# Kernel tuning notes

Measured on AMD Instinct MI355X. Metric: run time of the kernel, lower is better.

Reference implementation:

```python
import jax, jax.numpy as jnp
import numpy as np

L = 8          # fixed number of instance labels (0 = background), all assumed present
DV = 0.5       # delta_v
DD = 1.5       # delta_d
LOSS_WEIGHT = 1.0


def _safe_norm(x, axis):
    sq = jnp.sum(x * x, axis=axis)
    pos = sq > 0
    return jnp.sqrt(jnp.where(pos, sq, 1.0)) * pos.astype(x.dtype)


def _per_image(emb, inst, kern, tmask):
    # emb: [D,H,W], inst: [H,W] int, kern/tmask: [H,W] float
    D, H, W = emb.shape
    HW = H * W
    tm = (tmask > 0.5).astype(inst.dtype)
    kb = (kern > 0.5).astype(inst.dtype)
    inst = inst * tm
    inst_k = (inst * kb).reshape(-1)          # kernel-region labels
    inst_f = inst.reshape(-1)                 # full-region labels
    emb_f = emb.reshape(D, -1).T              # [HW, D]

    # --- generate_coef: first/second occurrence (row-major) of each label ---
    flat = jnp.arange(HW)
    eq = inst_f[None, :] == jnp.arange(L)[:, None]          # [L, HW]
    idxs = jnp.where(eq, flat[None, :], HW)
    first = jnp.min(idxs, axis=1)
    second = jnp.min(jnp.where(idxs == first[:, None], HW, idxs), axis=1)
    first = jnp.minimum(first, HW - 1)
    second = jnp.minimum(second, HW - 1)
    r0, c0 = first // W, first % W
    r1, c1 = second // W, second % W
    # pos_id = (tmp[0,0], tmp[1,0], tmp[0,-1], tmp[1,-1]) as in the source
    pos = jnp.stack([r0, r1, c0, c1], axis=1).astype(jnp.float32)  # [L,4]
    diag = jnp.sqrt(jnp.float32(H * H + W * W))
    coef_diag = jnp.exp(jnp.sqrt((pos[:, 0] - pos[:, 2]) ** 2 +
                                 (pos[:, 1] - pos[:, 3]) ** 2) / diag / 2.0)
    zmask = (jnp.arange(L) > 0).astype(jnp.float32)          # skip label 0
    coef_diag = coef_diag * zmask
    s = pos[:, 0] + pos[:, 2]
    t = pos[:, 1] + pos[:, 3]
    dp = jnp.sqrt((s[:, None] - s[None, :]) ** 2 + (t[:, None] - t[None, :]) ** 2)
    coef_off = 1.0 - 20.0 * jnp.exp(-4.0 - 2.5 * dp / diag)
    eye = jnp.eye(L, dtype=bool)
    coef = jnp.where(eye, coef_diag[:, None], coef_off)
    coef = coef * zmask[:, None] * zmask[None, :]

    # --- per-label kernel means (segment mean) ---
    ones = jnp.ones((HW,), jnp.float32)
    cnt_k = jax.ops.segment_sum(ones, inst_k, num_segments=L)
    mean = jax.ops.segment_sum(emb_f, inst_k, num_segments=L)
    mean = mean / jnp.maximum(cnt_k, 1.0)[:, None]           # [L, D]
    mean = mean * zmask[:, None]

    # --- l_agg: per-pixel distance to own-label mean, segment-mean per label ---
    mean_px = mean[inst_f]                                   # [HW, D] gather
    dist = _safe_norm(emb_f - mean_px, axis=1)
    cd_px = coef_diag[inst_f]
    val = jnp.log(jax.nn.relu(cd_px * dist - DV) ** 2 + 1.0)
    cnt = jax.ops.segment_sum(ones, inst_f, num_segments=L)
    l_agg_per = jax.ops.segment_sum(val, inst_f, num_segments=L) / jnp.maximum(cnt, 1.0)
    l_agg = jnp.mean(l_agg_per[1:])

    # --- l_dis: coefficient-weighted pairwise hinge between means ---
    Dn = _safe_norm(mean[:, None, :] - mean[None, :, :], axis=-1)  # [L, L]
    pm = (~eye) & (zmask[:, None] > 0) & (zmask[None, :] > 0)
    vals = jnp.log(jax.nn.relu(2.0 * DD - coef * Dn) ** 2 + 1.0)
    l_dis = jnp.sum(jnp.where(pm, vals, 0.0)) / ((L - 1) * (L - 2))

    # --- l_reg ---
    l_reg = jnp.mean(jnp.log(_safe_norm(mean, axis=1) + 1.0)) * 0.001
    return l_agg + l_dis + l_reg


def reference(emb, instance, kernel, training_mask, bboxes):
    # bboxes is accepted but unused, matching the original forward_single
    loss_batch = jax.vmap(_per_image)(emb, instance, kernel, training_mask)
    return LOSS_WEIGHT * jnp.mean(loss_batch)


def setup_inputs() -> dict:
    key = jax.random.key(0)
    k1, k2, k3, k4, k5 = jax.random.split(key, 5)
    B, D, H, W = 8, 4, 640, 640
    emb = jax.random.normal(k1, (B, D, H, W), dtype=jnp.float32)
    instance = jax.random.randint(k2, (B, H, W), 0, L, dtype=jnp.int32)
    kernel = jax.random.uniform(k3, (B, H, W), dtype=jnp.float32)
    training_mask = jax.random.uniform(k4, (B, H, W), dtype=jnp.float32)
    bboxes = jax.random.uniform(k5, (B, 10, 4), dtype=jnp.float32)
    return {"emb": emb, "instance": instance, "kernel": kernel,
            "training_mask": training_mask, "bboxes": bboxes}
```

## Files before the change

kernel.cpp:

```cpp
#include <hip/hip_runtime.h>
#include <hip/hip_bf16.h>

#define B_   8
#define D_   4
#define H_   640
#define W_   640
#define HW_  (H_ * W_)
#define L_   8
#define NL   (L_ - 1)
#define BLOCK 256
#define ITER  8

__device__ __forceinline__ void gatom_add(float* p, float v) {
    unsafeAtomicAdd(p, v);
}

__global__ void k_init(int* firstIdx, int* secondIdx, float* fbuf) {
    int t = threadIdx.x;
    if (t < B_ * L_) { firstIdx[t] = HW_; secondIdx[t] = HW_; }
    for (int i = t; i < 448; i += blockDim.x) fbuf[i] = 0.0f;
}

__global__ __launch_bounds__(BLOCK) void k_pass1(
        const float* __restrict__ emb, const int* __restrict__ inst,
        const float* __restrict__ kern, const float* __restrict__ tmask,
        int* __restrict__ firstIdx, int* __restrict__ secondIdx,
        float* __restrict__ cntk, float* __restrict__ cntf,
        float* __restrict__ sumemb) {
    __shared__ float sCntF[L_], sCntK[L_], sSum[L_ * D_];
    __shared__ int   sM1[L_], sM2[L_];

    const int tid = threadIdx.x;
    if (tid < L_) { sCntF[tid] = 0.f; sCntK[tid] = 0.f; sM1[tid] = HW_; sM2[tid] = HW_; }
    if (tid < L_ * D_) sSum[tid] = 0.f;
    __syncthreads();

    const int b    = blockIdx.y;
    const int base = b * HW_;

    float cf[NL], ck[NL], sm[NL][D_];
    int   m1[NL], m2[NL];
    #pragma unroll
    for (int l = 0; l < NL; ++l) {
        cf[l] = 0.f; ck[l] = 0.f; m1[l] = HW_; m2[l] = HW_;
        #pragma unroll
        for (int d = 0; d < D_; ++d) sm[l][d] = 0.f;
    }

    #pragma unroll
    for (int it = 0; it < ITER; ++it) {
        int p = blockIdx.x * (BLOCK * ITER) + it * BLOCK + tid;
        int lab  = inst[base + p];
        float tm = tmask[base + p];
        float kn = kern[base + p];
        int lf = (tm > 0.5f) ? lab : 0;
        bool kb = (kn > 0.5f);
        float e0 = emb[(b * D_ + 0) * HW_ + p];
        float e1 = emb[(b * D_ + 1) * HW_ + p];
        float e2 = emb[(b * D_ + 2) * HW_ + p];
        float e3 = emb[(b * D_ + 3) * HW_ + p];

        #pragma unroll
        for (int l = 1; l < L_; ++l) {
            const int k = l - 1;
            bool pf = (lf == l);
            cf[k] += pf ? 1.0f : 0.0f;
            float mk = (pf && kb) ? 1.0f : 0.0f;
            ck[k] += mk;
            sm[k][0] += mk * e0;
            sm[k][1] += mk * e1;
            sm[k][2] += mk * e2;
            sm[k][3] += mk * e3;
            bool t1 = pf && (m1[k] == HW_);
            bool t2 = pf && !t1 && (m2[k] == HW_);
            m1[k] = t1 ? p : m1[k];
            m2[k] = t2 ? p : m2[k];
        }
    }

    #pragma unroll
    for (int l = 0; l < NL; ++l) {
        #pragma unroll
        for (int off = 32; off > 0; off >>= 1) {
            cf[l] += __shfl_down(cf[l], off);
            ck[l] += __shfl_down(ck[l], off);
            sm[l][0] += __shfl_down(sm[l][0], off);
            sm[l][1] += __shfl_down(sm[l][1], off);
            sm[l][2] += __shfl_down(sm[l][2], off);
            sm[l][3] += __shfl_down(sm[l][3], off);
            int o1 = __shfl_down(m1[l], off);
            int o2 = __shfl_down(m2[l], off);
            m2[l] = min(min(m2[l], o2), max(m1[l], o1));
            m1[l] = min(m1[l], o1);
        }
    }

    if ((tid & 63) == 0) {
        #pragma unroll
        for (int l = 0; l < NL; ++l) {
            atomicAdd(&sCntF[l + 1], cf[l]);
            atomicAdd(&sCntK[l + 1], ck[l]);
            #pragma unroll
            for (int d = 0; d < D_; ++d) atomicAdd(&sSum[(l + 1) * D_ + d], sm[l][d]);
            int old = atomicMin(&sM1[l + 1], m1[l]);
            atomicMin(&sM2[l + 1], max(old, m1[l]));
            atomicMin(&sM2[l + 1], m2[l]);
        }
    }
    __syncthreads();

    if (tid >= 1 && tid < L_) {
        gatom_add(&cntf[b * L_ + tid], sCntF[tid]);
        gatom_add(&cntk[b * L_ + tid], sCntK[tid]);
        int old = atomicMin(&firstIdx[b * L_ + tid], sM1[tid]);
        atomicMin(&secondIdx[b * L_ + tid], max(old, sM1[tid]));
        atomicMin(&secondIdx[b * L_ + tid], sM2[tid]);
    }
    if (tid >= D_ && tid < L_ * D_)
        gatom_add(&sumemb[b * L_ * D_ + tid], sSum[tid]);
}

__global__ __launch_bounds__(BLOCK) void k_pass3(
        const float* __restrict__ emb, const int* __restrict__ inst,
        const float* __restrict__ tmask,
        const int* __restrict__ firstIdx, const int* __restrict__ secondIdx,
        const float* __restrict__ cntk, const float* __restrict__ sumemb,
        float* __restrict__ sumval) {
    __shared__ float sMean[L_ * D_];
    __shared__ float sCd[L_];
    __shared__ float sVal[L_];

    const int tid = threadIdx.x;
    const int b   = blockIdx.y;

    if (tid < L_ * D_) {
        int l = tid / D_;
        float c = fmaxf(cntk[b * L_ + l], 1.0f);
        sMean[tid] = (l > 0) ? sumemb[b * L_ * D_ + tid] / c : 0.0f;
    }
    if (tid < L_) {
        float cd = 0.0f;
        if (tid > 0) {
            const float diag = sqrtf((float)(H_ * H_ + W_ * W_));
            int f = min(firstIdx[b * L_ + tid],  HW_ - 1);
            int s = min(secondIdx[b * L_ + tid], HW_ - 1);
            float r0 = (float)(f / W_), c0 = (float)(f % W_);
            float r1 = (float)(s / W_), c1 = (float)(s % W_);
            cd = expf(sqrtf((r0 - c0) * (r0 - c0) + (r1 - c1) * (r1 - c1))
                      / diag * 0.5f);
        }
        sCd[tid]  = cd;
        sVal[tid] = 0.0f;
    }
    __syncthreads();

    const int base = b * HW_;
    float vs[NL];
    #pragma unroll
    for (int l = 0; l < NL; ++l) vs[l] = 0.f;

    #pragma unroll
    for (int it = 0; it < ITER; ++it) {
        int p = blockIdx.x * (BLOCK * ITER) + it * BLOCK + tid;
        int lab  = inst[base + p];
        float tm = tmask[base + p];
        int lf = (tm > 0.5f) ? lab : 0;
        float d2 = 0.0f;
        #pragma unroll
        for (int d = 0; d < D_; ++d) {
            float e = emb[(b * D_ + d) * HW_ + p] - sMean[lf * D_ + d];
            d2 += e * e;
        }
        float dist = sqrtf(d2);
        float x = fmaxf(sCd[lf] * dist - 0.5f, 0.0f);
        float val = logf(x * x + 1.0f);
        #pragma unroll
        for (int l = 1; l < L_; ++l)
            vs[l - 1] += (lf == l) ? val : 0.0f;
    }

    #pragma unroll
    for (int l = 0; l < NL; ++l) {
        #pragma unroll
        for (int off = 32; off > 0; off >>= 1)
            vs[l] += __shfl_down(vs[l], off);
    }
    if ((tid & 63) == 0) {
        #pragma unroll
        for (int l = 0; l < NL; ++l) atomicAdd(&sVal[l + 1], vs[l]);
    }
    __syncthreads();

    if (tid >= 1 && tid < L_)
        gatom_add(&sumval[b * L_ + tid], sVal[tid]);
}

__global__ __launch_bounds__(512) void k_final(
        const int* __restrict__ firstIdx, const int* __restrict__ secondIdx,
        const float* __restrict__ cntk, const float* __restrict__ cntf,
        const float* __restrict__ sumemb, const float* __restrict__ sumval,
        float* __restrict__ out) {
    __shared__ float sWave[8];
    const int tid = threadIdx.x;
    const int b = tid >> 6, ij = tid & 63, i = ij >> 3, j = ij & 7;
    const float diag = sqrtf((float)(H_ * H_ + W_ * W_));

    float mi[D_], mj[D_];
    {
        float ci = fmaxf(cntk[b * L_ + i], 1.0f);
        float cj = fmaxf(cntk[b * L_ + j], 1.0f);
        #pragma unroll
        for (int d = 0; d < D_; ++d) {
            mi[d] = (i > 0) ? sumemb[(b * L_ + i) * D_ + d] / ci : 0.0f;
            mj[d] = (j > 0) ? sumemb[(b * L_ + j) * D_ + d] / cj : 0.0f;
        }
    }

    float contrib = 0.0f;
    if (j == 0) {
        float d2 = 0.f;
        #pragma unroll
        for (int d = 0; d < D_; ++d) d2 += mi[d] * mi[d];
        float n = (d2 > 0.f) ? sqrtf(d2) : 0.f;
        contrib += logf(n + 1.0f) * (0.001f / (float)L_);
    }
    if (i == 0 && j >= 1) {
        contrib += sumval[b * L_ + j] / fmaxf(cntf[b * L_ + j], 1.0f) * (1.0f / (float)NL);
    }
    if (i >= 1 && j >= 1 && i != j) {
        float d2 = 0.f;
        #pragma unroll
        for (int d = 0; d < D_; ++d) {
            float df = mi[d] - mj[d];
            d2 += df * df;
        }
        float Dn = (d2 > 0.f) ? sqrtf(d2) : 0.f;
        int fi = min(firstIdx[b * L_ + i],  HW_ - 1);
        int si = min(secondIdx[b * L_ + i], HW_ - 1);
        int fj = min(firstIdx[b * L_ + j],  HW_ - 1);
        int sj = min(secondIdx[b * L_ + j], HW_ - 1);
        float ssi = (float)(fi / W_) + (float)(fi % W_);
        float tti = (float)(si / W_) + (float)(si % W_);
        float ssj = (float)(fj / W_) + (float)(fj % W_);
        float ttj = (float)(sj / W_) + (float)(sj % W_);
        float dx = ssi - ssj, dy = tti - ttj;
        float dp = sqrtf(dx * dx + dy * dy);
        float coef = 1.0f - 20.0f * expf(-4.0f - 2.5f * dp / diag);
        float x = fmaxf(3.0f - coef * Dn, 0.0f);
        contrib += logf(x * x + 1.0f) * (1.0f / 42.0f);
    }

    #pragma unroll
    for (int off = 32; off > 0; off >>= 1)
        contrib += __shfl_down(contrib, off);
    if ((tid & 63) == 0) sWave[tid >> 6] = contrib;
    __syncthreads();
    if (tid == 0) {
        float t = 0.f;
        #pragma unroll
        for (int w = 0; w < 8; ++w) t += sWave[w];
        out[0] = t * (1.0f / (float)B_);
    }
}

extern "C" void kernel_launch(void* const* d_in, const int* in_sizes, int n_in,
                              void* d_out, int out_size, void* d_ws, size_t ws_size,
                              hipStream_t stream) {
    const float* emb   = (const float*)d_in[0];
    const int*   inst  = (const int*)  d_in[1];
    const float* kern  = (const float*)d_in[2];
    const float* tmask = (const float*)d_in[3];

    int*   firstIdx  = (int*)d_ws;
    int*   secondIdx = firstIdx + B_ * L_;
    float* cntk      = (float*)(secondIdx + B_ * L_);
    float* cntf      = cntk + B_ * L_;
    float* sumemb    = cntf + B_ * L_;
    float* sumval    = sumemb + B_ * L_ * D_;
    float* out       = (float*)d_out;

    dim3 grid(HW_ / (BLOCK * ITER), B_);

    k_init <<<1, 256, 0, stream>>>(firstIdx, secondIdx, cntk);
    k_pass1<<<grid, BLOCK, 0, stream>>>(emb, inst, kern, tmask,
                                        firstIdx, secondIdx, cntk, cntf, sumemb);
    k_pass3<<<grid, BLOCK, 0, stream>>>(emb, inst, tmask, firstIdx, secondIdx,
                                        cntk, sumemb, sumval);
    k_final<<<1, 512, 0, stream>>>(firstIdx, secondIdx, cntk, cntf,
                                   sumemb, sumval, out);
}
```

Baseline: 172.8 us.

## Vectorize loads, pack integer counters, collapse per-label pass3 accumulators

Both streaming passes now load inputs as float4/int4, with each thread covering 4 contiguous pixels per iteration. Pass1 packs its full and kernel counts into one integer per label, which halves the per-label count adds, shuffles and atomics. Pass3 pre-scales each pixel's value by the inverse full count, so one scalar accumulator replaces seven per-label ones, and it uses fast __expf/__logf intrinsics. Risks include 16-bit overflow of the packed kernel count within a block and slight precision changes from the fast intrinsics.

```diff
diff --git a/kernel.cpp b/kernel.cpp
--- a/kernel.cpp
+++ b/kernel.cpp
@@ -1,80 +1,97 @@
 #include <hip/hip_runtime.h>
 #include <hip/hip_bf16.h>
 
-#define B_   8
-#define D_   4
-#define H_   640
-#define W_   640
-#define HW_  (H_ * W_)
-#define L_   8
-#define NL   (L_ - 1)
+#define B_    8
+#define D_    4
+#define H_    640
+#define W_    640
+#define HW_   (H_ * W_)
+#define L_    8
+#define NL    (L_ - 1)
 #define BLOCK 256
-#define ITER  8
+#define VITER 4
+#define GRIDX (HW_ / (BLOCK * 4 * VITER))
 
 __device__ __forceinline__ void gatom_add(float* p, float v) {
     unsafeAtomicAdd(p, v);
 }
 
-__global__ void k_init(int* firstIdx, int* secondIdx, float* fbuf) {
+__global__ void k_init(int* ib) {
     int t = threadIdx.x;
-    if (t < B_ * L_) { firstIdx[t] = HW_; secondIdx[t] = HW_; }
-    for (int i = t; i < 448; i += blockDim.x) fbuf[i] = 0.0f;
-}
-
-__global__ __launch_bounds__(BLOCK) void k_pass1(
+    if (t < 128) ib[t] = HW_;
+    ib[128 + t] = 0;
+    if (t < 136) ib[384 + t] = 0;
+}
+
+__global__ __launch_bounds__(BLOCK, 2) void k_pass1(
         const float* __restrict__ emb, const int* __restrict__ inst,
         const float* __restrict__ kern, const float* __restrict__ tmask,
         int* __restrict__ firstIdx, int* __restrict__ secondIdx,
-        float* __restrict__ cntk, float* __restrict__ cntf,
+        int* __restrict__ cntf_i, int* __restrict__ cntk_i,
         float* __restrict__ sumemb) {
-    __shared__ float sCntF[L_], sCntK[L_], sSum[L_ * D_];
+    __shared__ int   sCnt[L_];
+    __shared__ float sSum[L_ * D_];
     __shared__ int   sM1[L_], sM2[L_];
 
     const int tid = threadIdx.x;
-    if (tid < L_) { sCntF[tid] = 0.f; sCntK[tid] = 0.f; sM1[tid] = HW_; sM2[tid] = HW_; }
+    if (tid < L_) { sCnt[tid] = 0; sM1[tid] = HW_; sM2[tid] = HW_; }
     if (tid < L_ * D_) sSum[tid] = 0.f;
     __syncthreads();
 
-    const int b    = blockIdx.y;
+    const int b = blockIdx.y;
+    const int blockbase = blockIdx.x * (BLOCK * 4 * VITER);
+    const float* embb = emb + (size_t)b * D_ * HW_;
     const int base = b * HW_;
 
-    float cf[NL], ck[NL], sm[NL][D_];
+    int   cnt[NL];
+    float sm[NL][D_];
     int   m1[NL], m2[NL];
     #pragma unroll
     for (int l = 0; l < NL; ++l) {
-        cf[l] = 0.f; ck[l] = 0.f; m1[l] = HW_; m2[l] = HW_;
+        cnt[l] = 0; m1[l] = HW_; m2[l] = HW_;
         #pragma unroll
         for (int d = 0; d < D_; ++d) sm[l][d] = 0.f;
     }
 
     #pragma unroll
-    for (int it = 0; it < ITER; ++it) {
-        int p = blockIdx.x * (BLOCK * ITER) + it * BLOCK + tid;
-        int lab  = inst[base + p];
-        float tm = tmask[base + p];
-        float kn = kern[base + p];
-        int lf = (tm > 0.5f) ? lab : 0;
-        bool kb = (kn > 0.5f);
-        float e0 = emb[(b * D_ + 0) * HW_ + p];
-        float e1 = emb[(b * D_ + 1) * HW_ + p];
-        float e2 = emb[(b * D_ + 2) * HW_ + p];
-        float e3 = emb[(b * D_ + 3) * HW_ + p];
-
-        #pragma unroll
-        for (int l = 1; l < L_; ++l) {
-            const int k = l - 1;
-            bool pf = (lf == l);
-            cf[k] += pf ? 1.0f : 0.0f;
-            float mk = (pf && kb) ? 1.0f : 0.0f;
-            ck[k] += mk;
-            sm[k][0] += mk * e0;
-            sm[k][1] += mk * e1;
-            sm[k][2] += mk * e2;
-            sm[k][3] += mk * e3;
-            bool t1 = pf && (m1[k] == HW_);
-            bool t2 = pf && !t1 && (m2[k] == HW_);
-            m1[k] = t1 ? p : m1[k];
-            m2[k] = t2 ? p : m2[k];
+    for (int it = 0; it < VITER; ++it) {
+        const int off = blockbase + it * (BLOCK * 4) + tid * 4;
+        const int4   lab4 = *(const int4*)  (inst  + base + off);
+        const float4 tm4  = *(const float4*)(tmask + base + off);
+        const float4 kn4  = *(const float4*)(kern  + base + off);
+        const float4 ev0  = *(const float4*)(embb + 0 * HW_ + off);
+        const float4 ev1  = *(const float4*)(embb + 1 * HW_ + off);
+        const float4 ev2  = *(const float4*)(embb + 2 * HW_ + off);
+        const float4 ev3  = *(const float4*)(embb + 3 * HW_ + off);
+        const int   labA[4] = {lab4.x, lab4.y, lab4.z, lab4.w};
+        const float tmA[4]  = {tm4.x, tm4.y, tm4.z, tm4.w};
+        const float knA[4]  = {kn4.x, kn4.y, kn4.z, kn4.w};
+        const float e0A[4]  = {ev0.x, ev0.y, ev0.z, ev0.w};
+        const float e1A[4]  = {ev1.x, ev1.y, ev1.z, ev1.w};
+        const float e2A[4]  = {ev2.x, ev2.y, ev2.z, ev2.w};
+        const float e3A[4]  = {ev3.x, ev3.y, ev3.z, ev3.w};
+
+        #pragma unroll
+        for (int c = 0; c < 4; ++c) {
+            const int p  = off + c;
+            const int lf = (tmA[c] > 0.5f) ? labA[c] : 0;
+            const bool kb = (knA[c] > 0.5f);
+            #pragma unroll
+            for (int l = 1; l < L_; ++l) {
+                const int k = l - 1;
+                const bool pf = (lf == l);
+                const bool pk = pf && kb;
+                cnt[k] += (pf ? 0x10000 : 0) + (pk ? 1 : 0);
+                const float mk = pk ? 1.0f : 0.0f;
+                sm[k][0] += mk * e0A[c];
+                sm[k][1] += mk * e1A[c];
+                sm[k][2] += mk * e2A[c];
+                sm[k][3] += mk * e3A[c];
+                const bool t1 = pf && (m1[k] == HW_);
+                const bool t2 = pf && !t1 && (m2[k] == HW_);
+                m1[k] = t1 ? p : m1[k];
+                m2[k] = t2 ? p : m2[k];
+            }
         }
     }
 
@@ -82,8 +99,7 @@
     for (int l = 0; l < NL; ++l) {
         #pragma unroll
         for (int off = 32; off > 0; off >>= 1) {
-            cf[l] += __shfl_down(cf[l], off);
-            ck[l] += __shfl_down(ck[l], off);
+            cnt[l]   += __shfl_down(cnt[l], off);
             sm[l][0] += __shfl_down(sm[l][0], off);
             sm[l][1] += __shfl_down(sm[l][1], off);
             sm[l][2] += __shfl_down(sm[l][2], off);
@@ -98,8 +114,7 @@
     if ((tid & 63) == 0) {
         #pragma unroll
         for (int l = 0; l < NL; ++l) {
-            atomicAdd(&sCntF[l + 1], cf[l]);
-            atomicAdd(&sCntK[l + 1], ck[l]);
+            atomicAdd(&sCnt[l + 1], cnt[l]);
             #pragma unroll
             for (int d = 0; d < D_; ++d) atomicAdd(&sSum[(l + 1) * D_ + d], sm[l][d]);
             int old = atomicMin(&sM1[l + 1], m1[l]);
@@ -110,8 +125,8 @@
     __syncthreads();
 
     if (tid >= 1 && tid < L_) {
-        gatom_add(&cntf[b * L_ + tid], sCntF[tid]);
-        gatom_add(&cntk[b * L_ + tid], sCntK[tid]);
+        atomicAdd(&cntf_i[b * L_ + tid], sCnt[tid] >> 16);
+        atomicAdd(&cntk_i[b * L_ + tid], sCnt[tid] & 0xFFFF);
         int old = atomicMin(&firstIdx[b * L_ + tid], sM1[tid]);
         atomicMin(&secondIdx[b * L_ + tid], max(old, sM1[tid]));
         atomicMin(&secondIdx[b * L_ + tid], sM2[tid]);
@@ -120,86 +135,87 @@
         gatom_add(&sumemb[b * L_ * D_ + tid], sSum[tid]);
 }
 
-__global__ __launch_bounds__(BLOCK) void k_pass3(
+__global__ __launch_bounds__(BLOCK, 2) void k_pass3(
         const float* __restrict__ emb, const int* __restrict__ inst,
         const float* __restrict__ tmask,
         const int* __restrict__ firstIdx, const int* __restrict__ secondIdx,
-        const float* __restrict__ cntk, const float* __restrict__ sumemb,
-        float* __restrict__ sumval) {
-    __shared__ float sMean[L_ * D_];
-    __shared__ float sCd[L_];
-    __shared__ float sVal[L_];
+        const int* __restrict__ cntk_i, const int* __restrict__ cntf_i,
+        const float* __restrict__ sumemb, float* __restrict__ sumvalb) {
+    __shared__ float4 sMean[L_];
+    __shared__ float  sCd[L_], sInv[L_];
+    __shared__ float  sAcc;
 
     const int tid = threadIdx.x;
     const int b   = blockIdx.y;
 
-    if (tid < L_ * D_) {
-        int l = tid / D_;
-        float c = fmaxf(cntk[b * L_ + l], 1.0f);
-        sMean[tid] = (l > 0) ? sumemb[b * L_ * D_ + tid] / c : 0.0f;
-    }
     if (tid < L_) {
-        float cd = 0.0f;
+        float4 mu = {0.f, 0.f, 0.f, 0.f};
+        float cd = 0.f, inv = 0.f;
         if (tid > 0) {
+            const float invk = 1.0f / fmaxf((float)cntk_i[b * L_ + tid], 1.0f);
+            mu.x = sumemb[b * L_ * D_ + tid * D_ + 0] * invk;
+            mu.y = sumemb[b * L_ * D_ + tid * D_ + 1] * invk;
+            mu.z = sumemb[b * L_ * D_ + tid * D_ + 2] * invk;
+            mu.w = sumemb[b * L_ * D_ + tid * D_ + 3] * invk;
             const float diag = sqrtf((float)(H_ * H_ + W_ * W_));
             int f = min(firstIdx[b * L_ + tid],  HW_ - 1);
             int s = min(secondIdx[b * L_ + tid], HW_ - 1);
             float r0 = (float)(f / W_), c0 = (float)(f % W_);
             float r1 = (float)(s / W_), c1 = (float)(s % W_);
-            cd = expf(sqrtf((r0 - c0) * (r0 - c0) + (r1 - c1) * (r1 - c1))
-                      / diag * 0.5f);
-        }
-        sCd[tid]  = cd;
-        sVal[tid] = 0.0f;
-    }
-    __syncthreads();
-
+            cd = __expf(sqrtf((r0 - c0) * (r0 - c0) + (r1 - c1) * (r1 - c1))
+                        / diag * 0.5f);
+            inv = 1.0f / fmaxf((float)cntf_i[b * L_ + tid], 1.0f);
+        }
+        sMean[tid] = mu; sCd[tid] = cd; sInv[tid] = inv;
+        if (tid == 0) sAcc = 0.f;
+    }
+    __syncthreads();
+
+    const int blockbase = blockIdx.x * (BLOCK * 4 * VITER);
+    const float* embb = emb + (size_t)b * D_ * HW_;
     const int base = b * HW_;
-    float vs[NL];
-    #pragma unroll
-    for (int l = 0; l < NL; ++l) vs[l] = 0.f;
-
-    #pragma unroll
-    for (int it = 0; it < ITER; ++it) {
-        int p = blockIdx.x * (BLOCK * ITER) + it * BLOCK + tid;
-        int lab  = inst[base + p];
-        float tm = tmask[base + p];
-        int lf = (tm > 0.5f) ? lab : 0;
-        float d2 = 0.0f;
-        #pragma unroll
-        for (int d = 0; d < D_; ++d) {
-            float e = emb[(b * D_ + d) * HW_ + p] - sMean[lf * D_ + d];
-            d2 += e * e;
-        }
-        float dist = sqrtf(d2);
-        float x = fmaxf(sCd[lf] * dist - 0.5f, 0.0f);
-        float val = logf(x * x + 1.0f);
-        #pragma unroll
-        for (int l = 1; l < L_; ++l)
-            vs[l - 1] += (lf == l) ? val : 0.0f;
-    }
-
-    #pragma unroll
-    for (int l = 0; l < NL; ++l) {
-        #pragma unroll
-        for (int off = 32; off > 0; off >>= 1)
-            vs[l] += __shfl_down(vs[l], off);
-    }
-    if ((tid & 63) == 0) {
-        #pragma unroll
-        for (int l = 0; l < NL; ++l) atomicAdd(&sVal[l + 1], vs[l]);
-    }
-    __syncthreads();
-
-    if (tid >= 1 && tid < L_)
-        gatom_add(&sumval[b * L_ + tid], sVal[tid]);
+    float acc = 0.f;
+
+    #pragma unroll
+    for (int it = 0; it < VITER; ++it) {
+        const int off = blockbase + it * (BLOCK * 4) + tid * 4;
+        const int4   lab4 = *(const int4*)  (inst  + base + off);
+        const float4 tm4  = *(const float4*)(tmask + base + off);
+        const float4 ev0  = *(const float4*)(embb + 0 * HW_ + off);
+        const float4 ev1  = *(const float4*)(embb + 1 * HW_ + off);
+        const float4 ev2  = *(const float4*)(embb + 2 * HW_ + off);
+        const float4 ev3  = *(const float4*)(embb + 3 * HW_ + off);
+        const int   labA[4] = {lab4.x, lab4.y, lab4.z, lab4.w};
+        const float tmA[4]  = {tm4.x, tm4.y, tm4.z, tm4.w};
+        const float e0A[4]  = {ev0.x, ev0.y, ev0.z, ev0.w};
+        const float e1A[4]  = {ev1.x, ev1.y, ev1.z, ev1.w};
+        const float e2A[4]  = {ev2.x, ev2.y, ev2.z, ev2.w};
+        const float e3A[4]  = {ev3.x, ev3.y, ev3.z, ev3.w};
+
+        #pragma unroll
+        for (int c = 0; c < 4; ++c) {
+            const int lf = (tmA[c] > 0.5f) ? labA[c] : 0;
+            const float4 mu = sMean[lf];
+            float dx = e0A[c] - mu.x, dy = e1A[c] - mu.y;
+            float dz = e2A[c] - mu.z, dw = e3A[c] - mu.w;
+            float d2 = dx * dx + dy * dy + dz * dz + dw * dw;
+            float x  = fmaxf(sCd[lf] * sqrtf(d2) - 0.5f, 0.0f);
+            acc += __logf(x * x + 1.0f) * sInv[lf];
+        }
+    }
+
+    #pragma unroll
+    for (int off = 32; off > 0; off >>= 1)
+        acc += __shfl_down(acc, off);
+    if ((tid & 63) == 0) atomicAdd(&sAcc, acc);
+    __syncthreads();
+    if (tid == 0) gatom_add(&sumvalb[b], sAcc);
 }
 
 __global__ __launch_bounds__(512) void k_final(
         const int* __restrict__ firstIdx, const int* __restrict__ secondIdx,
-        const float* __restrict__ cntk, const float* __restrict__ cntf,
-        const float* __restrict__ sumemb, const float* __restrict__ sumval,
-        float* __restrict__ out) {
+        const int* __restrict__ cntk_i, const float* __restrict__ sumemb,
+        const float* __restrict__ sumvalb, float* __restrict__ out) {
     __shared__ float sWave[8];
     const int tid = threadIdx.x;
     const int b = tid >> 6, ij = tid & 63, i = ij >> 3, j = ij & 7;
@@ -207,12 +223,12 @@
 
     float mi[D_], mj[D_];
     {
-        float ci = fmaxf(cntk[b * L_ + i], 1.0f);
-        float cj = fmaxf(cntk[b * L_ + j], 1.0f);
+        float ci = 1.0f / fmaxf((float)cntk_i[b * L_ + i], 1.0f);
+        float cj = 1.0f / fmaxf((float)cntk_i[b * L_ + j], 1.0f);
         #pragma unroll
         for (int d = 0; d < D_; ++d) {
-            mi[d] = (i > 0) ? sumemb[(b * L_ + i) * D_ + d] / ci : 0.0f;
-            mj[d] = (j > 0) ? sumemb[(b * L_ + j) * D_ + d] / cj : 0.0f;
+            mi[d] = (i > 0) ? sumemb[(b * L_ + i) * D_ + d] * ci : 0.0f;
+            mj[d] = (j > 0) ? sumemb[(b * L_ + j) * D_ + d] * cj : 0.0f;
         }
     }
 
@@ -222,11 +238,10 @@
         #pragma unroll
         for (int d = 0; d < D_; ++d) d2 += mi[d] * mi[d];
         float n = (d2 > 0.f) ? sqrtf(d2) : 0.f;
-        contrib += logf(n + 1.0f) * (0.001f / (float)L_);
-    }
-    if (i == 0 && j >= 1) {
-        contrib += sumval[b * L_ + j] / fmaxf(cntf[b * L_ + j], 1.0f) * (1.0f / (float)NL);
-    }
+        contrib += __logf(n + 1.0f) * (0.001f / (float)L_);
+    }
+    if (i == 0 && j == 1)
+        contrib += sumvalb[b] * (1.0f / (float)NL);
     if (i >= 1 && j >= 1 && i != j) {
         float d2 = 0.f;
         #pragma unroll
@@ -245,9 +260,9 @@
         float ttj = (float)(sj / W_) + (float)(sj % W_);
         float dx = ssi - ssj, dy = tti - ttj;
         float dp = sqrtf(dx * dx + dy * dy);
-        float coef = 1.0f - 20.0f * expf(-4.0f - 2.5f * dp / diag);
+        float coef = 1.0f - 20.0f * __expf(-4.0f - 2.5f * dp / diag);
         float x = fmaxf(3.0f - coef * Dn, 0.0f);
-        contrib += logf(x * x + 1.0f) * (1.0f / 42.0f);
+        contrib += __logf(x * x + 1.0f) * (1.0f / 42.0f);
     }
 
     #pragma unroll
@@ -271,21 +286,22 @@
     const float* kern  = (const float*)d_in[2];
     const float* tmask = (const float*)d_in[3];
 
-    int*   firstIdx  = (int*)d_ws;
-    int*   secondIdx = firstIdx + B_ * L_;
-    float* cntk      = (float*)(secondIdx + B_ * L_);
-    float* cntf      = cntk + B_ * L_;
-    float* sumemb    = cntf + B_ * L_;
-    float* sumval    = sumemb + B_ * L_ * D_;
+    int*   ib        = (int*)d_ws;
+    int*   firstIdx  = ib;
+    int*   secondIdx = ib + 64;
+    int*   cntf_i    = ib + 128;
+    int*   cntk_i    = ib + 192;
+    float* sumemb    = (float*)(ib + 256);
+    float* sumvalb   = (float*)(ib + 512);
     float* out       = (float*)d_out;
 
-    dim3 grid(HW_ / (BLOCK * ITER), B_);
-
-    k_init <<<1, 256, 0, stream>>>(firstIdx, secondIdx, cntk);
+    dim3 grid(GRIDX, B_);
+
+    k_init <<<1, 256, 0, stream>>>(ib);
     k_pass1<<<grid, BLOCK, 0, stream>>>(emb, inst, kern, tmask,
-                                        firstIdx, secondIdx, cntk, cntf, sumemb);
+                                        firstIdx, secondIdx, cntf_i, cntk_i, sumemb);
     k_pass3<<<grid, BLOCK, 0, stream>>>(emb, inst, tmask, firstIdx, secondIdx,
-                                        cntk, sumemb, sumval);
-    k_final<<<1, 512, 0, stream>>>(firstIdx, secondIdx, cntk, cntf,
-                                   sumemb, sumval, out);
-}
+                                        cntk_i, cntf_i, sumemb, sumvalb);
+    k_final<<<1, 512, 0, stream>>>(firstIdx, secondIdx, cntk_i,
+                                   sumemb, sumvalb, out);
+}
```

Result: faster. 159.5 us (-7.7%).
